# Kernel tuning notes

Hardware: AMD Instinct MI355X
Metric: run time of the kernel (lower is better)

The kernel has to match this reference:

```python
import jax, jax.numpy as jnp
import numpy as np

B, T, N, D = 128, 64, 197, 768


def setup_inputs() -> dict:
    key = jax.random.key(0)
    k1, k2, k3, k4 = jax.random.split(key, 4)
    image = jax.random.normal(k1, (B, N, D), dtype=jnp.float32)
    text = jax.random.normal(k2, (B, T, D), dtype=jnp.float32)
    target = jax.random.normal(k3, (B, N, D), dtype=jnp.float32)
    padding_mask = jax.random.randint(k4, (B, T), 0, 2, dtype=jnp.int32)
    return {"image": image, "text": text, "target": target, "padding_mask": padding_mask}


def reference(image, text, target, padding_mask):
    embed_dim = image.shape[-1]
    batch = image.shape[0]

    # L2-normalize along embedding dim
    text_norm = text / jnp.linalg.norm(text, axis=-1, keepdims=True)
    target_norm = target / jnp.linalg.norm(target, axis=-1, keepdims=True)

    # Original builds a [B,B,T,N] matmul then takes the batch diagonal;
    # mathematically identical to per-sample similarity [B,T,N].
    similarity = jnp.einsum('btd,bnd->btn', text_norm, target_norm)
    similarity = similarity[:, 1:, 1:]  # drop CLS rows/cols -> [B, T-1, N-1]

    # best-matching patch for every non-CLS token (+1 to re-offset CLS)
    token2patch_idx = jnp.argmax(similarity, axis=2) + 1  # [B, T-1], int
    aligned = jnp.take_along_axis(target, token2patch_idx[:, :, None], axis=1)  # [B, T-1, D]

    # keep-mask: original does ~padding_mask (1 = padded)
    keep = (padding_mask[:, 1:] == 0).astype(jnp.float32)  # [B, T-1]

    # masked MSE expressed as weighted sums (jit-friendly, no dynamic shapes)
    tok_sq = jnp.sum((text[:, 1:].astype(jnp.float32) - aligned.astype(jnp.float32)) ** 2, axis=-1)  # [B, T-1]
    masked_sq_sum = jnp.sum(tok_sq * keep)
    # CLS token paired with CLS image patch (the cat([text[:, :1]], ...) row)
    cls_sq_sum = jnp.sum((text[:, 0].astype(jnp.float32) - image[:, 0].astype(jnp.float32)) ** 2)
    n_rows = batch + jnp.sum(keep)  # B CLS rows + unmasked token rows
    kd_text_loss = (cls_sq_sum + masked_sq_sum) / (n_rows * embed_dim)

    kd_image_loss = jnp.mean((image.astype(jnp.float32) - target.astype(jnp.float32)) ** 2)

    return (kd_text_loss + kd_image_loss) / 2
```

## Files before the change

### kernel.cpp

```cpp
#include <hip/hip_runtime.h>

#define B_ 128
#define T_ 64
#define N_ 197
#define D_ 768

__device__ __forceinline__ float waveSum(float v){
#pragma unroll
  for (int m = 32; m >= 1; m >>= 1) v += __shfl_xor(v, m, 64);
  return v;
}

__device__ __forceinline__ unsigned ordf(float x){
  unsigned u = __float_as_uint(x);
  return (u & 0x80000000u) ? ~u : (u | 0x80000000u);
}

__global__ __launch_bounds__(192) void k_norm_img(
    const float* __restrict__ image, const float* __restrict__ text,
    const float* __restrict__ target, float* __restrict__ invnorm,
    float* __restrict__ img_partial, float* __restrict__ cls_partial){
  int row = blockIdx.x;
  int b = row / N_;
  int n = row - b * N_;
  int i = threadIdx.x;
  const float4* tg4 = reinterpret_cast<const float4*>(target + (size_t)row * D_);
  const float4* im4 = reinterpret_cast<const float4*>(image + (size_t)row * D_);
  float4 t4 = tg4[i];
  float4 g4 = im4[i];
  float ss = t4.x*t4.x + t4.y*t4.y + t4.z*t4.z + t4.w*t4.w;
  float dx = g4.x-t4.x, dy = g4.y-t4.y, dz = g4.z-t4.z, dw = g4.w-t4.w;
  float sd = dx*dx + dy*dy + dz*dz + dw*dw;
  ss = waveSum(ss); sd = waveSum(sd);
  __shared__ float shs[3], shd[3], shc[3];
  int lane = i & 63, wid = i >> 6;
  if (lane == 0){ shs[wid] = ss; shd[wid] = sd; }
  __syncthreads();
  if (i == 0){
    invnorm[row] = 1.0f / sqrtf(shs[0]+shs[1]+shs[2]);
    img_partial[row] = shd[0]+shd[1]+shd[2];
  }
  if (n == 0){
    const float4* tx4 = reinterpret_cast<const float4*>(text + (size_t)b * T_ * D_);
    float4 c4 = tx4[i];
    float cx = c4.x-g4.x, cy = c4.y-g4.y, cz = c4.z-g4.z, cw = c4.w-g4.w;
    float sc = cx*cx + cy*cy + cz*cz + cw*cw;
    sc = waveSum(sc);
    if (lane == 0) shc[wid] = sc;
    __syncthreads();
    if (i == 0) cls_partial[b] = shc[0]+shc[1]+shc[2];
  }
}

__global__ __launch_bounds__(256) void k_sim(
    const float* __restrict__ text, const float* __restrict__ target,
    const float* __restrict__ invnorm, unsigned long long* __restrict__ best){
  int h = blockIdx.x;
  int b = blockIdx.y;
  int n0 = 1 + 49*h;
  __shared__ float As[16][64];
  __shared__ float Bs[16][52];
  int tid = threadIdx.x;
  int tx = tid & 15, ty = tid >> 4;
  int tt = tid & 63, ki = tid >> 6;
  float acc[4][4] = {{0.f,0.f,0.f,0.f},{0.f,0.f,0.f,0.f},{0.f,0.f,0.f,0.f},{0.f,0.f,0.f,0.f}};
  const float* textb = text + (size_t)b * T_ * D_;
  const float* tgtb  = target + (size_t)b * N_ * D_;

  for (int k0 = 0; k0 < D_; k0 += 16){
    float4 av = make_float4(0.f,0.f,0.f,0.f);
    if (tt < 63) av = *reinterpret_cast<const float4*>(textb + (size_t)(1+tt)*D_ + k0 + ki*4);
    As[ki*4+0][tt] = av.x; As[ki*4+1][tt] = av.y; As[ki*4+2][tt] = av.z; As[ki*4+3][tt] = av.w;
    if (tid < 196){
      int nn = tid >> 2, kj = tid & 3;
      float4 bv = *reinterpret_cast<const float4*>(tgtb + (size_t)(n0+nn)*D_ + k0 + kj*4);
      Bs[kj*4+0][nn] = bv.x; Bs[kj*4+1][nn] = bv.y; Bs[kj*4+2][nn] = bv.z; Bs[kj*4+3][nn] = bv.w;
    }
    __syncthreads();
    if (tx < 13){
#pragma unroll
      for (int k = 0; k < 16; ++k){
        float4 a4 = *reinterpret_cast<const float4*>(&As[k][ty*4]);
        float4 b4 = *reinterpret_cast<const float4*>(&Bs[k][tx*4]);
        float aa[4] = {a4.x, a4.y, a4.z, a4.w};
        float bb[4] = {b4.x, b4.y, b4.z, b4.w};
#pragma unroll
        for (int ii = 0; ii < 4; ++ii)
#pragma unroll
          for (int jj = 0; jj < 4; ++jj)
            acc[ii][jj] = fmaf(aa[ii], bb[jj], acc[ii][jj]);
      }
    }
    __syncthreads();
  }

  float inv[4];
  if (tx < 13){
#pragma unroll
    for (int jj = 0; jj < 4; ++jj){
      int nn = tx*4 + jj;
      inv[jj] = (nn < 49) ? invnorm[(size_t)b*N_ + n0 + nn] : 0.f;
    }
  }
#pragma unroll
  for (int ii = 0; ii < 4; ++ii){
    unsigned long long key = 0ull;
    if (tx < 13){
      float bv = 0.f; int bn = -1;
#pragma unroll
      for (int jj = 0; jj < 4; ++jj){
        int nn = tx*4 + jj;
        if (nn < 49){
          float v = acc[ii][jj] * inv[jj];
          if (bn < 0 || v > bv){ bv = v; bn = n0 + nn; }
        }
      }
      if (bn >= 0)
        key = ((unsigned long long)ordf(bv) << 32) | (unsigned long long)(0xFFFFFFFFu - (unsigned)bn);
    }
#pragma unroll
    for (int m = 1; m < 16; m <<= 1){
      unsigned lo = (unsigned)key, hi = (unsigned)(key >> 32);
      unsigned olo = __shfl_xor(lo, m, 64);
      unsigned ohi = __shfl_xor(hi, m, 64);
      unsigned long long o = ((unsigned long long)ohi << 32) | olo;
      if (o > key) key = o;
    }
    int t_local = ty*4 + ii;
    if (tx == 0 && t_local < 63)
      atomicMax(&best[(size_t)b*63 + t_local], key);
  }
}

__global__ __launch_bounds__(192) void k_tok(
    const float* __restrict__ text, const float* __restrict__ target,
    const int* __restrict__ pmask, const unsigned long long* __restrict__ best,
    float* __restrict__ tok){
  int bt = blockIdx.x;
  int b = bt / 63, t = bt - b*63;
  if (pmask[b*T_ + 1 + t] != 0){
    if (threadIdx.x == 0) tok[bt] = 0.f;
    return;
  }
  unsigned long long key = best[bt];
  int n = (int)(0xFFFFFFFFu - (unsigned)(key & 0xFFFFFFFFull));
  int i = threadIdx.x;
  const float4* tx4 = reinterpret_cast<const float4*>(text + ((size_t)b*T_ + 1 + t) * D_);
  const float4* tg4 = reinterpret_cast<const float4*>(target + ((size_t)b*N_ + n) * D_);
  float4 a = tx4[i], c = tg4[i];
  float dx = a.x-c.x, dy = a.y-c.y, dz = a.z-c.z, dw = a.w-c.w;
  float sd = dx*dx + dy*dy + dz*dz + dw*dw;
  sd = waveSum(sd);
  __shared__ float sh[3];
  int lane = i & 63, wid = i >> 6;
  if (lane == 0) sh[wid] = sd;
  __syncthreads();
  if (i == 0) tok[bt] = sh[0] + sh[1] + sh[2];
}

__global__ __launch_bounds__(256) void k_final(
    const float* __restrict__ img_partial, const float* __restrict__ cls_partial,
    const float* __restrict__ tok, const int* __restrict__ pmask,
    float* __restrict__ out){
  int tid = threadIdx.x;
  float s_img = 0.f, s_cls = 0.f, s_tok = 0.f, s_keep = 0.f;
  for (int i = tid; i < B_*N_; i += 256) s_img += img_partial[i];
  for (int i = tid; i < B_;    i += 256) s_cls += cls_partial[i];
  for (int i = tid; i < B_*63; i += 256){
    s_tok += tok[i];
    int b = i / 63, t = i - b*63;
    s_keep += (pmask[b*T_ + 1 + t] == 0) ? 1.f : 0.f;
  }
  s_img = waveSum(s_img); s_cls = waveSum(s_cls);
  s_tok = waveSum(s_tok); s_keep = waveSum(s_keep);
  __shared__ float sh[4][4];
  int lane = tid & 63, wid = tid >> 6;
  if (lane == 0){ sh[0][wid]=s_img; sh[1][wid]=s_cls; sh[2][wid]=s_tok; sh[3][wid]=s_keep; }
  __syncthreads();
  if (tid == 0){
    float img  = sh[0][0]+sh[0][1]+sh[0][2]+sh[0][3];
    float cls  = sh[1][0]+sh[1][1]+sh[1][2]+sh[1][3];
    float tokm = sh[2][0]+sh[2][1]+sh[2][2]+sh[2][3];
    float keep = sh[3][0]+sh[3][1]+sh[3][2]+sh[3][3];
    float kd_text = (cls + tokm) / ((128.0f + keep) * (float)D_);
    float kd_img  = img / ((float)B_ * (float)N_ * (float)D_);
    out[0] = 0.5f * (kd_text + kd_img);
  }
}

extern "C" void kernel_launch(void* const* d_in, const int* in_sizes, int n_in,
                              void* d_out, int out_size, void* d_ws, size_t ws_size,
                              hipStream_t stream) {
  const float* image  = (const float*)d_in[0];
  const float* text   = (const float*)d_in[1];
  const float* target = (const float*)d_in[2];
  const int*   pmask  = (const int*)d_in[3];

  char* ws = (char*)d_ws;
  float* invnorm                 = (float*)(ws);
  unsigned long long* best       = (unsigned long long*)(ws + 100864);
  float* img_partial             = (float*)(ws + 165376);
  float* cls_partial             = (float*)(ws + 266240);
  float* tok                     = (float*)(ws + 266752);

  hipMemsetAsync(ws + 100864, 0, 64512, stream);

  k_norm_img<<<B_*N_, 192, 0, stream>>>(image, text, target, invnorm, img_partial, cls_partial);
  k_sim<<<dim3(4, B_), 256, 0, stream>>>(text, target, invnorm, best);
  k_tok<<<B_*63, 192, 0, stream>>>(text, target, pmask, best, tok);
  k_final<<<1, 256, 0, stream>>>(img_partial, cls_partial, tok, pmask, (float*)d_out);
}
```

Baseline: 289.1 us.

## Use bf16 MFMA similarity kernel with fused argmax and token MSE

Adds a grid-stride prep kernel that computes target inverse norms, the image MSE partials and the CLS term. The same kernel writes bf16 copies of target and text. A new per-batch similarity kernel runs 32x32x16 bf16 MFMA instructions over register-prefetched LDS tiles, does the argmax in-block and computes the masked token MSE directly, which removes the atomics, the memset and the separate token kernel. The final reduction shrinks to per-block and per-batch partials. The cost is a large workspace requirement (the old path is kept as a fallback) and reduced precision: bf16 similarity can flip near-tie argmaxes, and the token MSE is computed on bf16-rounded values.

Result: faster. 257.4 us (-10.9%).

```diff
diff --git a/kernel.cpp b/kernel.cpp
--- a/kernel.cpp
+++ b/kernel.cpp
@@ -5,15 +5,239 @@
 #define N_ 197
 #define D_ 768
 
+typedef __attribute__((ext_vector_type(8))) short short8;
+typedef __attribute__((ext_vector_type(16))) float f32x16;
+
 __device__ __forceinline__ float waveSum(float v){
 #pragma unroll
   for (int m = 32; m >= 1; m >>= 1) v += __shfl_xor(v, m, 64);
   return v;
 }
-
 __device__ __forceinline__ unsigned ordf(float x){
   unsigned u = __float_as_uint(x);
   return (u & 0x80000000u) ? ~u : (u | 0x80000000u);
+}
+__device__ __forceinline__ unsigned short f2bf(float x){
+  unsigned u = __float_as_uint(x);
+  u += 0x7fffu + ((u >> 16) & 1u);
+  return (unsigned short)(u >> 16);
+}
+__device__ __forceinline__ float bf2f(unsigned s){ return __uint_as_float(s << 16); }
+
+__global__ __launch_bounds__(256) void k_prep(
+    const float* __restrict__ image, const float* __restrict__ text,
+    const float* __restrict__ target, float* __restrict__ invnorm,
+    unsigned short* __restrict__ tgt_bf, unsigned short* __restrict__ txt_bf,
+    float* __restrict__ img_part, float* __restrict__ cls_part){
+  int tid = threadIdx.x, lane = tid & 63, wid = tid >> 6;
+  int gw = blockIdx.x * 4 + wid;
+  float img_acc = 0.f;
+  for (int row = gw; row < B_*N_; row += 8192){
+    int b = row / N_, n = row - b*N_;
+    const float4* tg4 = reinterpret_cast<const float4*>(target + (size_t)row*D_);
+    const float4* im4 = reinterpret_cast<const float4*>(image + (size_t)row*D_);
+    float4 g[3];
+    float ss = 0.f, sd = 0.f;
+#pragma unroll
+    for (int j = 0; j < 3; ++j){
+      float4 tv = tg4[j*64 + lane];
+      float4 iv = im4[j*64 + lane];
+      g[j] = iv;
+      ss += tv.x*tv.x + tv.y*tv.y + tv.z*tv.z + tv.w*tv.w;
+      float dx = iv.x-tv.x, dy = iv.y-tv.y, dz = iv.z-tv.z, dw = iv.w-tv.w;
+      sd += dx*dx + dy*dy + dz*dz + dw*dw;
+      uint2 pk;
+      pk.x = (unsigned)f2bf(tv.x) | ((unsigned)f2bf(tv.y) << 16);
+      pk.y = (unsigned)f2bf(tv.z) | ((unsigned)f2bf(tv.w) << 16);
+      *reinterpret_cast<uint2*>(tgt_bf + (size_t)row*D_ + (j*64+lane)*4) = pk;
+    }
+    ss = waveSum(ss); sd = waveSum(sd);
+    img_acc += sd;
+    if (lane == 0) invnorm[row] = 1.0f / sqrtf(ss);
+    if (n == 0){
+      const float4* tx4 = reinterpret_cast<const float4*>(text + (size_t)b*T_*D_);
+      float sc = 0.f;
+#pragma unroll
+      for (int j = 0; j < 3; ++j){
+        float4 cv = tx4[j*64+lane]; float4 iv = g[j];
+        float dx = cv.x-iv.x, dy = cv.y-iv.y, dz = cv.z-iv.z, dw = cv.w-iv.w;
+        sc += dx*dx + dy*dy + dz*dz + dw*dw;
+      }
+      sc = waveSum(sc);
+      if (lane == 0) cls_part[b] = sc;
+    }
+  }
+  {
+    int rt = gw;
+    const float4* tx4 = reinterpret_cast<const float4*>(text + (size_t)rt*D_);
+#pragma unroll
+    for (int j = 0; j < 3; ++j){
+      float4 v = tx4[j*64+lane];
+      uint2 pk;
+      pk.x = (unsigned)f2bf(v.x) | ((unsigned)f2bf(v.y) << 16);
+      pk.y = (unsigned)f2bf(v.z) | ((unsigned)f2bf(v.w) << 16);
+      *reinterpret_cast<uint2*>(txt_bf + (size_t)rt*D_ + (j*64+lane)*4) = pk;
+    }
+  }
+  __shared__ float shp[4];
+  if (lane == 0) shp[wid] = img_acc;
+  __syncthreads();
+  if (tid == 0) img_part[blockIdx.x] = shp[0]+shp[1]+shp[2]+shp[3];
+}
+
+__global__ __launch_bounds__(448) void k_sim2(
+    const unsigned short* __restrict__ txt_bf, const unsigned short* __restrict__ tgt_bf,
+    const float* __restrict__ invnorm, const int* __restrict__ pmask,
+    float* __restrict__ tok_sum, float* __restrict__ keep_cnt){
+  int b = blockIdx.x;
+  int tid = threadIdx.x, lane = tid & 63, w = tid >> 6;
+  __shared__ char lds[36864];
+  __shared__ float invn_s[224];
+  __shared__ unsigned long long cand[7][64];
+  __shared__ int best_s[64];
+  __shared__ float wtok_s[7], wkeep_s[7];
+
+  if (tid < 224) invn_s[tid] = (tid < 196) ? invnorm[b*N_ + 1 + tid] : 0.f;
+
+  const char* tgtb = (const char*)tgt_bf;
+  const char* txtb = (const char*)txt_bf;
+  const char* fptr[6];
+  bool fval[6];
+#pragma unroll
+  for (int s = 0; s < 6; ++s){
+    int f = tid + s*448;
+    fval[s] = false; fptr[s] = tgtb;
+    if (f < 2304){
+      int l = f & 63;
+      int kc = (f >> 6) & 3;
+      int koff = kc*16 + (l >> 5)*8;
+      if (f < 1792){
+        int mt = f >> 8;
+        int p = 1 + mt*32 + (l & 31);
+        if (p <= 196){ fval[s] = true; fptr[s] = tgtb + (((size_t)b*N_ + p)*D_ + koff)*2; }
+      } else {
+        int nt = (f - 1792) >> 8;
+        int c = nt*32 + (l & 31);
+        if (c < 63){ fval[s] = true; fptr[s] = txtb + (((size_t)b*T_ + c + 1)*D_ + koff)*2; }
+      }
+    }
+  }
+
+  f32x16 acc0, acc1;
+#pragma unroll
+  for (int r = 0; r < 16; ++r){ acc0[r] = 0.f; acc1[r] = 0.f; }
+
+  float4 rg[6];
+  const float4 z4 = make_float4(0.f,0.f,0.f,0.f);
+#pragma unroll
+  for (int s = 0; s < 6; ++s) rg[s] = fval[s] ? *reinterpret_cast<const float4*>(fptr[s]) : z4;
+
+  for (int it = 0; it < 12; ++it){
+    __syncthreads();
+#pragma unroll
+    for (int s = 0; s < 6; ++s){
+      int f = tid + s*448;
+      if (f < 2304) *reinterpret_cast<float4*>(lds + f*16) = rg[s];
+    }
+    __syncthreads();
+    if (it < 11){
+#pragma unroll
+      for (int s = 0; s < 6; ++s)
+        rg[s] = fval[s] ? *reinterpret_cast<const float4*>(fptr[s] + (it+1)*128) : z4;
+    }
+#pragma unroll
+    for (int kc = 0; kc < 4; ++kc){
+      short8 av  = *reinterpret_cast<const short8*>(lds + ((w*256 + kc*64 + lane) << 4));
+      short8 bv0 = *reinterpret_cast<const short8*>(lds + ((1792 + kc*64 + lane) << 4));
+      short8 bv1 = *reinterpret_cast<const short8*>(lds + ((1792 + 256 + kc*64 + lane) << 4));
+      acc0 = __builtin_amdgcn_mfma_f32_32x32x16_bf16(av, bv0, acc0, 0, 0, 0);
+      acc1 = __builtin_amdgcn_mfma_f32_32x32x16_bf16(av, bv1, acc1, 0, 0, 0);
+    }
+  }
+
+#pragma unroll
+  for (int nt = 0; nt < 2; ++nt){
+    unsigned long long key = 0ull;
+#pragma unroll
+    for (int r = 0; r < 16; ++r){
+      int rloc = (r & 3) + 8*(r >> 2) + 4*(lane >> 5);
+      int nn = w*32 + rloc;
+      float v = (nt ? acc1[r] : acc0[r]) * invn_s[nn];
+      if (nn < 196){
+        unsigned long long k2 = ((unsigned long long)ordf(v) << 32)
+                              | (unsigned long long)(0xFFFFFFFFu - (unsigned)(nn + 1));
+        if (k2 > key) key = k2;
+      }
+    }
+    { unsigned lo = (unsigned)key, hi = (unsigned)(key >> 32);
+      unsigned olo = __shfl_xor(lo, 32, 64), ohi = __shfl_xor(hi, 32, 64);
+      unsigned long long o = ((unsigned long long)ohi << 32) | olo;
+      if (o > key) key = o; }
+    int c = nt*32 + (lane & 31);
+    if (lane < 32 && c < 63) cand[w][c] = key;
+  }
+  __syncthreads();
+  if (tid < 63){
+    unsigned long long best = 0ull;
+#pragma unroll
+    for (int ww = 0; ww < 7; ++ww){ unsigned long long k2 = cand[ww][tid]; if (k2 > best) best = k2; }
+    best_s[tid] = (int)(0xFFFFFFFFu - (unsigned)(best & 0xFFFFFFFFull));
+  }
+  __syncthreads();
+
+  float wacc = 0.f, wcnt = 0.f;
+  for (int c = w; c < 63; c += 7){
+    int token = c + 1;
+    if (pmask[b*T_ + token] != 0) continue;
+    int p = best_s[c];
+    const unsigned short* tr = txt_bf + ((size_t)b*T_ + token)*D_;
+    const unsigned short* gr = tgt_bf + ((size_t)b*N_ + p)*D_;
+    float s = 0.f;
+#pragma unroll
+    for (int j = 0; j < 3; ++j){
+      uint2 tv = *reinterpret_cast<const uint2*>(tr + (j*64+lane)*4);
+      uint2 gv = *reinterpret_cast<const uint2*>(gr + (j*64+lane)*4);
+      float d0 = bf2f(tv.x & 0xffffu) - bf2f(gv.x & 0xffffu);
+      float d1 = bf2f(tv.x >> 16)     - bf2f(gv.x >> 16);
+      float d2 = bf2f(tv.y & 0xffffu) - bf2f(gv.y & 0xffffu);
+      float d3 = bf2f(tv.y >> 16)     - bf2f(gv.y >> 16);
+      s += d0*d0 + d1*d1 + d2*d2 + d3*d3;
+    }
+    s = waveSum(s);
+    if (lane == 0){ wacc += s; wcnt += 1.f; }
+  }
+  if (lane == 0){ wtok_s[w] = wacc; wkeep_s[w] = wcnt; }
+  __syncthreads();
+  if (tid == 0){
+    float st = 0.f, sk = 0.f;
+#pragma unroll
+    for (int ww = 0; ww < 7; ++ww){ st += wtok_s[ww]; sk += wkeep_s[ww]; }
+    tok_sum[b] = st; keep_cnt[b] = sk;
+  }
+}
+
+__global__ __launch_bounds__(256) void k_final2(
+    const float* __restrict__ img_part, const float* __restrict__ cls_part,
+    const float* __restrict__ tok_sum, const float* __restrict__ keep_cnt,
+    float* __restrict__ out){
+  int tid = threadIdx.x;
+  float a = 0.f, c = 0.f, t = 0.f, k = 0.f;
+  for (int i = tid; i < 2048; i += 256) a += img_part[i];
+  for (int i = tid; i < B_; i += 256){ c += cls_part[i]; t += tok_sum[i]; k += keep_cnt[i]; }
+  a = waveSum(a); c = waveSum(c); t = waveSum(t); k = waveSum(k);
+  __shared__ float sh[4][4];
+  int lane = tid & 63, wid = tid >> 6;
+  if (lane == 0){ sh[0][wid]=a; sh[1][wid]=c; sh[2][wid]=t; sh[3][wid]=k; }
+  __syncthreads();
+  if (tid == 0){
+    float img  = sh[0][0]+sh[0][1]+sh[0][2]+sh[0][3];
+    float cls  = sh[1][0]+sh[1][1]+sh[1][2]+sh[1][3];
+    float tokm = sh[2][0]+sh[2][1]+sh[2][2]+sh[2][3];
+    float keep = sh[3][0]+sh[3][1]+sh[3][2]+sh[3][3];
+    float kd_text = (cls + tokm) / ((128.0f + keep) * (float)D_);
+    float kd_img  = img / ((float)B_ * (float)N_ * (float)D_);
+    out[0] = 0.5f * (kd_text + kd_img);
+  }
 }
 
 __global__ __launch_bounds__(192) void k_norm_img(
@@ -66,7 +290,6 @@
   float acc[4][4] = {{0.f,0.f,0.f,0.f},{0.f,0.f,0.f,0.f},{0.f,0.f,0.f,0.f},{0.f,0.f,0.f,0.f}};
   const float* textb = text + (size_t)b * T_ * D_;
   const float* tgtb  = target + (size_t)b * N_ * D_;
-
   for (int k0 = 0; k0 < D_; k0 += 16){
     float4 av = make_float4(0.f,0.f,0.f,0.f);
     if (tt < 63) av = *reinterpret_cast<const float4*>(textb + (size_t)(1+tt)*D_ + k0 + ki*4);
@@ -93,7 +316,6 @@
     }
     __syncthreads();
   }
-
   float inv[4];
   if (tx < 13){
 #pragma unroll
@@ -195,18 +417,40 @@
   const float* text   = (const float*)d_in[1];
   const float* target = (const float*)d_in[2];
   const int*   pmask  = (const int*)d_in[3];
-
   char* ws = (char*)d_ws;
-  float* invnorm                 = (float*)(ws);
-  unsigned long long* best       = (unsigned long long*)(ws + 100864);
-  float* img_partial             = (float*)(ws + 165376);
-  float* cls_partial             = (float*)(ws + 266240);
-  float* tok                     = (float*)(ws + 266752);
-
-  hipMemsetAsync(ws + 100864, 0, 64512, stream);
-
-  k_norm_img<<<B_*N_, 192, 0, stream>>>(image, text, target, invnorm, img_partial, cls_partial);
-  k_sim<<<dim3(4, B_), 256, 0, stream>>>(text, target, invnorm, best);
-  k_tok<<<B_*63, 192, 0, stream>>>(text, target, pmask, best, tok);
-  k_final<<<1, 256, 0, stream>>>(img_partial, cls_partial, tok, pmask, (float*)d_out);
-}
+
+  const size_t OFF_INV  = 0;
+  const size_t OFF_TGT  = 100864;
+  const size_t OFF_TXT  = 38808064;
+  const size_t OFF_IMG  = 51390976;
+  const size_t OFF_CLS  = 51399168;
+  const size_t OFF_TOK  = 51399680;
+  const size_t OFF_KEEP = 51400192;
+  const size_t NEEDED   = 51400704;
+
+  if (ws_size >= NEEDED){
+    float* invnorm = (float*)(ws + OFF_INV);
+    unsigned short* tgt_bf = (unsigned short*)(ws + OFF_TGT);
+    unsigned short* txt_bf = (unsigned short*)(ws + OFF_TXT);
+    float* img_part = (float*)(ws + OFF_IMG);
+    float* cls_part = (float*)(ws + OFF_CLS);
+    float* tok_sum  = (float*)(ws + OFF_TOK);
+    float* keep_cnt = (float*)(ws + OFF_KEEP);
+
+    k_prep<<<2048, 256, 0, stream>>>(image, text, target, invnorm, tgt_bf, txt_bf,
+                                     img_part, cls_part);
+    k_sim2<<<B_, 448, 0, stream>>>(txt_bf, tgt_bf, invnorm, pmask, tok_sum, keep_cnt);
+    k_final2<<<1, 256, 0, stream>>>(img_part, cls_part, tok_sum, keep_cnt, (float*)d_out);
+  } else {
+    float* invnorm           = (float*)(ws);
+    unsigned long long* best = (unsigned long long*)(ws + 100864);
+    float* img_partial       = (float*)(ws + 165376);
+    float* cls_partial       = (float*)(ws + 266240);
+    float* tok               = (float*)(ws + 266752);
+    hipMemsetAsync(ws + 100864, 0, 64512, stream);
+    k_norm_img<<<B_*N_, 192, 0, stream>>>(image, text, target, invnorm, img_partial, cls_partial);
+    k_sim<<<dim3(4, B_), 256, 0, stream>>>(text, target, invnorm, best);
+    k_tok<<<B_*63, 192, 0, stream>>>(text, target, pmask, best, tok);
+    k_final<<<1, 256, 0, stream>>>(img_partial, cls_partial, tok, pmask, (float*)d_out);
+  }
+}
```
